# Kernel tuning notes

Measured on AMD Instinct MI355X. Metric: run time of the kernel, lower is better.

Reference implementation:

```python
import jax, jax.numpy as jnp
import numpy as np

# ---- module constants (from init_kwargs) ----
VOXEL_SIZE = np.array([0.1, 0.1, 0.2], np.float32)
PC_RANGE = np.array([0.0, -40.0, -3.0, 70.4, 40.0, 1.0], np.float32)
MAX_PTS = 10            # max_points_in_voxel
MAX_VOX = 40000         # max_voxel_num (hard voxelization cap per sample)
GRID = np.round((PC_RANGE[3:] - PC_RANGE[:3]) / VOXEL_SIZE).astype(np.int32)  # [704,800,20] (x,y,z)
BIG = int(GRID[0]) * int(GRID[1]) * int(GRID[2])

PC_MIN = jnp.asarray(PC_RANGE[:3])
VSIZE = jnp.asarray(VOXEL_SIZE)
GRID_J = jnp.asarray(GRID)

B = 8
N_PER_B = 120000


def setup_inputs() -> dict:
    key = jax.random.key(0)
    k1, = jax.random.split(key, 1)
    u = jax.random.uniform(k1, (B * N_PER_B, 4), dtype=jnp.float32)
    # place points inside (and slightly around) pc_range
    x = u[:, 0] * 72.0 - 0.5
    y = u[:, 1] * 82.0 - 41.0
    z = u[:, 2] * 4.4 - 3.2
    inten = u[:, 3]
    bs_idx = jnp.repeat(jnp.arange(B, dtype=jnp.float32), N_PER_B)
    points = jnp.stack([bs_idx, x, y, z, inten], axis=1)  # [960000, 5]
    return {"points": points, "batch_size": B}


def _voxelize_one(pts):
    """Hard voxelization of one point cloud pts [N,4] -> fixed-size buffers.
    Faithful to first-come voxel ordering and per-voxel point caps."""
    N = pts.shape[0]
    idxs = jnp.arange(N, dtype=jnp.int32)
    xyz = pts[:, :3]
    c = jnp.floor((xyz - PC_MIN) / VSIZE).astype(jnp.int32)  # [N,3] (x,y,z)
    valid = jnp.all((c >= 0) & (c < GRID_J), axis=1)
    lid = (c[:, 2] * GRID[1] + c[:, 1]) * GRID[0] + c[:, 0]  # z-major linear id
    lid = jnp.where(valid, lid, BIG)

    order = jnp.argsort(lid)            # stable: within a voxel, original order kept
    lid_s = lid[order]
    is_new = jnp.concatenate([jnp.ones((1,), bool), lid_s[1:] != lid_s[:-1]])
    gid = jnp.cumsum(is_new.astype(jnp.int32)) - 1           # group id per sorted point
    starts = jax.lax.cummax(jnp.where(is_new, idxs, 0))      # group start position
    pos = idxs - starts                                      # rank inside its voxel

    g_lid = jax.ops.segment_min(lid_s, gid, num_segments=N)
    g_valid = g_lid < BIG
    first_orig = jax.ops.segment_min(order.astype(jnp.int32), gid, num_segments=N)
    # voxel slot = first-appearance rank (invalid/empty groups pushed to the end)
    first_key = jnp.where(g_valid, first_orig, N + idxs)
    perm = jnp.argsort(first_key)
    slot = jnp.zeros(N, jnp.int32).at[perm].set(idxs)

    pslot = slot[gid]
    keep = g_valid[gid] & (pslot < MAX_VOX) & (pos < MAX_PTS)
    sslot = jnp.where(keep, pslot, MAX_VOX)   # overflow bucket, sliced off
    spos = jnp.where(keep, pos, 0)
    voxels = jnp.zeros((MAX_VOX + 1, MAX_PTS, pts.shape[1]), pts.dtype)
    voxels = voxels.at[sslot, spos].set(pts[order])[:MAX_VOX]

    gcount = jax.ops.segment_sum(keep.astype(jnp.int32), gid, num_segments=N)
    gslot = jnp.where(g_valid & (slot < MAX_VOX), slot, MAX_VOX)
    num_points = jnp.zeros(MAX_VOX + 1, jnp.int32).at[gslot].set(gcount)[:MAX_VOX]

    cs = c[order]
    gz = jax.ops.segment_min(cs[:, 2], gid, num_segments=N)
    gy = jax.ops.segment_min(cs[:, 1], gid, num_segments=N)
    gx = jax.ops.segment_min(cs[:, 0], gid, num_segments=N)
    coors = jnp.full((MAX_VOX + 1, 3), -1, jnp.int32)
    coors = coors.at[gslot].set(jnp.stack([gz, gy, gx], axis=1))[:MAX_VOX]  # (z,y,x)
    return voxels, num_points, coors


def reference(points, batch_size):
    feats = points[:, 1:]
    n_per_b = feats.shape[0] // batch_size  # points constructed contiguously per sample
    pts = feats.reshape(batch_size, n_per_b, feats.shape[1])
    voxels_b, num_b, coors_b = jax.vmap(_voxelize_one)(pts)
    voxels = voxels_b.reshape(batch_size * MAX_VOX, MAX_PTS, feats.shape[1])
    num_points = num_b.reshape(-1)
    batch_col = jnp.repeat(jnp.arange(batch_size, dtype=jnp.int32), MAX_VOX)[:, None]
    coors_batch = jnp.concatenate([batch_col, coors_b.reshape(-1, 3)], axis=1)  # [b,z,y,x]
    grid_size = jnp.asarray(GRID)
    return voxels, num_points, coors_batch, grid_size
```

## Files before the change

### kernel.cpp

```cpp
#include <hip/hip_runtime.h>

#define NB        8
#define NPB       120000
#define NPTS      (NB * NPB)
#define MAX_PTS   10
#define MAX_VOX   40000
#define GX        704
#define GY        800
#define GZ        20
#define CELLS     (GX * GY * GZ)
#define WPB       (CELLS / 32)

#define HC2       (1 << 15)
#define HMASK2    (HC2 - 1)
#define NSLOT2    (NB * HC2)

#define TILES     469
#define TILES_PAD 512
#define MBCAP     8192
#define MTILE     2048

#define EMPTY64   0xFFFFFFFFFFFFFFFFull

#define OUT_VOX   0LL
#define OUT_NUM   12800000LL
#define OUT_COOR  13120000LL
#define OUT_GRID  14400000LL

typedef float f4v __attribute__((ext_vector_type(4)));

__device__ __forceinline__ bool point_cell(const float* __restrict__ p,
                                           int& cx, int& cy, int& cz) {
    cx = (int)floorf((p[1] - 0.0f)   / 0.1f);
    cy = (int)floorf((p[2] - (-40.0f)) / 0.1f);
    cz = (int)floorf((p[3] - (-3.0f))  / 0.2f);
    return (cx >= 0) & (cx < GX) & (cy >= 0) & (cy < GY) & (cz >= 0) & (cz < GZ);
}

__device__ __forceinline__ unsigned cell_hash(int lid) {
    return (((unsigned)lid * 2654435761u) >> 17) & HMASK2;
}

__global__ void k_init(float* __restrict__ out, uint4* __restrict__ bm4,
                       ulonglong2* __restrict__ slab2, unsigned* __restrict__ mcount) {
    int t = blockIdx.x * blockDim.x + threadIdx.x;
    int stride = gridDim.x * blockDim.x;
    uint4 z4 = make_uint4(0u, 0u, 0u, 0u);
    for (int i = t; i < NB * WPB / 4; i += stride) bm4[i] = z4;
    ulonglong2 e2; e2.x = EMPTY64; e2.y = EMPTY64;
    if (t < NSLOT2 / 2) slab2[t] = e2;
    f4v z = {0.f, 0.f, 0.f, 0.f};
    f4v* vox = (f4v*)(out + OUT_VOX);
    for (int j = t; j < 3200000; j += stride)
        __builtin_nontemporal_store(z, vox + j);
    if (t < NB) mcount[t * 16] = 0u;
    if (t == 0) {
        out[OUT_GRID + 0] = 704.f;
        out[OUT_GRID + 1] = 800.f;
        out[OUT_GRID + 2] = 20.f;
    }
}

__global__ void k_phase1(const float* __restrict__ pts, unsigned* __restrict__ bm,
                         unsigned long long* __restrict__ slabB,
                         unsigned char* __restrict__ flag, int* __restrict__ lid32) {
    int b = blockIdx.x & 7;
    int idx = (blockIdx.x >> 3) * 256 + threadIdx.x;
    if (idx >= NPB) return;
    int g = b * NPB + idx;
    const float* p = pts + (long long)g * 5;
    int cx, cy, cz;
    if (!point_cell(p, cx, cy, cz)) { flag[g] = 0; lid32[g] = -1; return; }
    int lid = (cz * GY + cy) * GX + cx;
    lid32[g] = lid;
    unsigned mask = 1u << (lid & 31);
    unsigned old = atomicOr(&bm[b * WPB + (lid >> 5)], mask);
    if ((old & mask) == 0u) {
        flag[g] = 1;
    } else {
        flag[g] = 0;
        unsigned long long key = ((unsigned long long)(unsigned)lid << 32)
                               | (unsigned long long)(unsigned)idx;
        unsigned long long* base = slabB + (size_t)b * HC2;
        unsigned h = cell_hash(lid);
        while (true) {
            unsigned long long oo = atomicMin(base + h, key);
            if (oo == EMPTY64) break;
            if ((oo >> 32) == (key >> 32)) break;
            if (oo > key) key = oo;
            h = (h + 1) & HMASK2;
        }
    }
}

__global__ void k_phase2(const int* __restrict__ lid32, unsigned char* __restrict__ flag,
                         unsigned long long* __restrict__ slabB) {
    int b = blockIdx.x & 7;
    int idx = (blockIdx.x >> 3) * 256 + threadIdx.x;
    if (idx >= NPB) return;
    int g = b * NPB + idx;
    if (flag[g] != 1) return;
    int lid = lid32[g];
    unsigned long long* base = slabB + (size_t)b * HC2;
    unsigned h = cell_hash(lid);
    while (true) {
        unsigned long long cur = base[h];
        if (cur == EMPTY64) break;
        if ((unsigned)(cur >> 32) == (unsigned)lid) {
            unsigned long long key = ((unsigned long long)(unsigned)lid << 32)
                                   | (unsigned long long)(unsigned)idx;
            unsigned long long old = atomicMin(&base[h], key);
            unsigned omin = (unsigned)old;
            if (omin < (unsigned)idx) {
                flag[g] = 0;
                flag[b * NPB + (int)omin] = 1;
            }
            break;
        }
        h = (h + 1) & HMASK2;
    }
}

__global__ void k_count(const unsigned* __restrict__ flag32, int* __restrict__ tileSum) {
    int w = blockIdx.x * 4 + ((int)threadIdx.x >> 6);
    int lane = threadIdx.x & 63;
    int b = w & 7;
    int tile = w >> 3;
    int i = tile * 64 + lane;
    unsigned x = (i < NPB / 4) ? flag32[b * (NPB / 4) + i] : 0u;
    int s = (int)((x * 0x01010101u) >> 24);
    #pragma unroll
    for (int off = 32; off; off >>= 1) s += __shfl_down(s, off);
    if (lane == 0) tileSum[b * TILES_PAD + tile] = s;
}

__global__ void k_finish(const float* __restrict__ pts, const int* __restrict__ lid32,
                         const unsigned char* __restrict__ flag,
                         const int* __restrict__ tileSum,
                         const unsigned long long* __restrict__ slabB,
                         float* __restrict__ out, unsigned short* __restrict__ slotOf,
                         int2* __restrict__ mlist, unsigned* __restrict__ mcount) {
    int b = blockIdx.x & 7;
    int tile = blockIdx.x >> 3;
    int t = threadIdx.x;

    __shared__ int sc[256];
    __shared__ int soff[TILES_PAD];
    int v0 = (2 * t     < TILES) ? tileSum[b * TILES_PAD + 2 * t]     : 0;
    int v1 = (2 * t + 1 < TILES) ? tileSum[b * TILES_PAD + 2 * t + 1] : 0;
    int w = v0 + v1;
    sc[t] = w;
    __syncthreads();
    for (int off = 1; off < 256; off <<= 1) {
        int x = sc[t];
        if (t >= off) x += sc[t - off];
        __syncthreads();
        sc[t] = x;
        __syncthreads();
    }
    int e = sc[t] - w;
    soff[2 * t] = e;
    soff[2 * t + 1] = e + v0;
    __syncthreads();

    int idx = tile * 256 + t;
    int g = b * NPB + idx;
    int f = (idx < NPB) ? (int)flag[g] : 0;
    sc[t] = f;
    __syncthreads();
    for (int off = 1; off < 256; off <<= 1) {
        int x = sc[t];
        if (t >= off) x += sc[t - off];
        __syncthreads();
        sc[t] = x;
        __syncthreads();
    }
    int rank = sc[t] - f;

    if (idx >= NPB) return;
    int lid = lid32[g];
    if (lid < 0) return;

    if (f) {
        int slot = soff[tile] + rank;
        slotOf[g] = (unsigned short)(slot < 65535 ? slot : 65535);
        if (slot >= MAX_VOX) return;
        unsigned ul = (unsigned)lid;
        unsigned cx = ul % (unsigned)GX;
        unsigned tt = ul / (unsigned)GX;
        unsigned cy = tt % (unsigned)GY;
        unsigned cz = tt / (unsigned)GY;
        long long r = (long long)b * MAX_VOX + slot;
        ((float4*)(out + OUT_COOR))[r] = make_float4((float)b, (float)cz, (float)cy, (float)cx);
        out[OUT_NUM + r] = 1.f;
        const float* p = pts + (long long)g * 5;
        ((float4*)(out + OUT_VOX))[r * MAX_PTS] = make_float4(p[1], p[2], p[3], p[4]);
    } else {
        const unsigned long long* base = slabB + (size_t)b * HC2;
        unsigned h = cell_hash(lid);
        unsigned long long cur;
        while (true) {
            cur = base[h];
            if ((unsigned)(cur >> 32) == (unsigned)lid) break;
            h = (h + 1) & HMASK2;
        }
        unsigned minidx = (unsigned)cur;
        unsigned m = atomicAdd(&mcount[b * 16], 1u);
        if (m < MBCAP) mlist[(size_t)b * MBCAP + m] = make_int2((int)minidx, idx);
    }
}

__global__ void k_multi(const float* __restrict__ pts,
                        const int2* __restrict__ mlist, const unsigned* __restrict__ mcount,
                        const unsigned short* __restrict__ slotOf,
                        float* __restrict__ out) {
    int b = blockIdx.y;
    unsigned n = mcount[b * 16];
    if (n > MBCAP) n = MBCAP;
    unsigned t = blockIdx.x * blockDim.x + threadIdx.x;
    const int2* lst = mlist + (size_t)b * MBCAP;
    bool active = (t < n);
    int2 e = active ? lst[t] : make_int2(-1, -1);
    int pos = 1;
    int same = 0;
    __shared__ int2 sm[MTILE];
    for (unsigned chunk = 0; chunk < n; chunk += MTILE) {
        unsigned m = n - chunk;
        if (m > MTILE) m = MTILE;
        for (unsigned i = threadIdx.x; i < m; i += 256)
            sm[i] = lst[chunk + i];
        __syncthreads();
        if (active) {
            #pragma unroll 4
            for (unsigned j = 0; j < m; j++) {
                int2 o = sm[j];
                if (o.x == e.x) { same++; if (o.y < e.y) pos++; }
            }
        }
        __syncthreads();
    }
    if (!active) return;
    int slot = (int)slotOf[(size_t)b * NPB + e.x];
    if (slot >= MAX_VOX) return;
    if (pos == 1) {
        int cnt = same + 1;
        out[OUT_NUM + (long long)b * MAX_VOX + slot] =
            (float)(cnt < MAX_PTS ? cnt : MAX_PTS);
    }
    if (pos >= MAX_PTS) return;
    const float* p = pts + ((long long)b * NPB + e.y) * 5;
    ((float4*)(out + OUT_VOX))[(long long)(b * MAX_VOX + slot) * MAX_PTS + pos] =
        make_float4(p[1], p[2], p[3], p[4]);
}

extern "C" void kernel_launch(void* const* d_in, const int* in_sizes, int n_in,
                              void* d_out, int out_size, void* d_ws, size_t ws_size,
                              hipStream_t stream) {
    const float* pts = (const float*)d_in[0];
    float* out = (float*)d_out;

    char* w = (char*)d_ws;
    unsigned* bm = (unsigned*)w;              w += (size_t)NB * WPB * 4;
    unsigned long long* slabB = (unsigned long long*)w;
    w += (size_t)NSLOT2 * 8;
    int2* mlist = (int2*)w;  w += (size_t)NB * MBCAP * 8;
    int* lid32 = (int*)w;    w += (size_t)NPTS * 4;
    int* tileSum = (int*)w;  w += (size_t)NB * TILES_PAD * 4;
    unsigned* mcount = (unsigned*)w; w += (size_t)NB * 16 * 4;
    unsigned short* slotOf = (unsigned short*)w; w += (size_t)NPTS * 2;
    unsigned char* flag = (unsigned char*)w;  w += (size_t)NPTS;

    const int PB = TILES * NB;
    k_init<<<dim3(2048), dim3(256), 0, stream>>>(out, (uint4*)bm, (ulonglong2*)slabB, mcount);
    k_phase1<<<dim3(PB), dim3(256), 0, stream>>>(pts, bm, slabB, flag, lid32);
    k_phase2<<<dim3(PB), dim3(256), 0, stream>>>(lid32, flag, slabB);
    k_count<<<dim3((TILES * NB + 3) / 4), dim3(256), 0, stream>>>((const unsigned*)flag, tileSum);
    k_finish<<<dim3(PB), dim3(256), 0, stream>>>(pts, lid32, flag, tileSum, slabB,
                                                 out, slotOf, mlist, mcount);
    k_multi<<<dim3(MBCAP / 256, NB), dim3(256), 0, stream>>>(pts, mlist, mcount, slotOf, out);
}
```

Before: 164.1 us.

## Replace voxel occupancy bitmap with non-atomic two-level hash election tables

The full-grid occupancy bitmap and its atomicOr are replaced. Each valid point writes its index into a per-sample hash table with plain stores, and the surviving entry is checked against lid32 to pick one representative per cell. Colliding points go to a second, smaller table, and anything left over falls back to the existing atomicMin slab. This removes the large bitmap zeroing pass and most of the atomics. Cell computation is also folded into the init kernel. The cost is an extra kernel launch, scattered writes into about 10 MB of tables, and more complex flag-state logic in phase2.

```diff
diff --git a/kernel.cpp b/kernel.cpp
--- a/kernel.cpp
+++ b/kernel.cpp
@@ -8,8 +8,11 @@
 #define GX        704
 #define GY        800
 #define GZ        20
-#define CELLS     (GX * GY * GZ)
-#define WPB       (CELLS / 32)
+
+#define T0        (1 << 18)
+#define T0MASK    (T0 - 1)
+#define T1        (1 << 16)
+#define T1MASK    (T1 - 1)
 
 #define HC2       (1 << 15)
 #define HMASK2    (HC2 - 1)
@@ -37,22 +40,55 @@
     return (cx >= 0) & (cx < GX) & (cy >= 0) & (cy < GY) & (cz >= 0) & (cz < GZ);
 }
 
-__device__ __forceinline__ unsigned cell_hash(int lid) {
+__device__ __forceinline__ unsigned hash0(int lid) {
+    return (((unsigned)lid * 2654435761u) >> 14) & T0MASK;
+}
+__device__ __forceinline__ unsigned hash1(int lid) {
+    return (((unsigned)lid * 0x9E3779B1u) >> 16) & T1MASK;
+}
+__device__ __forceinline__ unsigned slab_hash(int lid) {
     return (((unsigned)lid * 2654435761u) >> 17) & HMASK2;
 }
 
-__global__ void k_init(float* __restrict__ out, uint4* __restrict__ bm4,
-                       ulonglong2* __restrict__ slab2, unsigned* __restrict__ mcount) {
-    int t = blockIdx.x * blockDim.x + threadIdx.x;
-    int stride = gridDim.x * blockDim.x;
-    uint4 z4 = make_uint4(0u, 0u, 0u, 0u);
-    for (int i = t; i < NB * WPB / 4; i += stride) bm4[i] = z4;
-    ulonglong2 e2; e2.x = EMPTY64; e2.y = EMPTY64;
-    if (t < NSLOT2 / 2) slab2[t] = e2;
+__device__ __forceinline__ void slab_insert(unsigned long long* __restrict__ base,
+                                            int lid, int idx) {
+    unsigned long long key = ((unsigned long long)(unsigned)lid << 32)
+                           | (unsigned long long)(unsigned)idx;
+    unsigned h = slab_hash(lid);
+    while (true) {
+        unsigned long long oo = atomicMin(base + h, key);
+        if (oo == EMPTY64) break;
+        if ((oo >> 32) == (key >> 32)) break;
+        if (oo > key) key = oo;
+        h = (h + 1) & HMASK2;
+    }
+}
+
+__global__ void k_init(const float* __restrict__ pts, float* __restrict__ out,
+                       ulonglong2* __restrict__ slab2, unsigned* __restrict__ tbl0,
+                       int* __restrict__ lid32, unsigned* __restrict__ mcount) {
+    int b = blockIdx.x & 7;
+    int idx = (blockIdx.x >> 3) * 256 + threadIdx.x;
+    if (idx < NPB) {
+        int g = b * NPB + idx;
+        const float* p = pts + (long long)g * 5;
+        int cx, cy, cz;
+        if (point_cell(p, cx, cy, cz)) {
+            int lid = (cz * GY + cy) * GX + cx;
+            lid32[g] = lid;
+            tbl0[b * T0 + hash0(lid)] = (unsigned)idx;
+        } else {
+            lid32[g] = -1;
+        }
+    }
+    int t = blockIdx.x * 256 + threadIdx.x;
+    int stride = gridDim.x * 256;
     f4v z = {0.f, 0.f, 0.f, 0.f};
     f4v* vox = (f4v*)(out + OUT_VOX);
     for (int j = t; j < 3200000; j += stride)
         __builtin_nontemporal_store(z, vox + j);
+    ulonglong2 e2; e2.x = EMPTY64; e2.y = EMPTY64;
+    if (t < NSLOT2 / 2) slab2[t] = e2;
     if (t < NB) mcount[t * 16] = 0u;
     if (t == 0) {
         out[OUT_GRID + 0] = 704.f;
@@ -61,63 +97,81 @@
     }
 }
 
-__global__ void k_phase1(const float* __restrict__ pts, unsigned* __restrict__ bm,
-                         unsigned long long* __restrict__ slabB,
-                         unsigned char* __restrict__ flag, int* __restrict__ lid32) {
+__global__ void k_l0(const int* __restrict__ lid32, const unsigned* __restrict__ tbl0,
+                     unsigned* __restrict__ tbl1, unsigned char* __restrict__ flag,
+                     unsigned long long* __restrict__ slabB) {
     int b = blockIdx.x & 7;
     int idx = (blockIdx.x >> 3) * 256 + threadIdx.x;
     if (idx >= NPB) return;
     int g = b * NPB + idx;
-    const float* p = pts + (long long)g * 5;
-    int cx, cy, cz;
-    if (!point_cell(p, cx, cy, cz)) { flag[g] = 0; lid32[g] = -1; return; }
-    int lid = (cz * GY + cy) * GX + cx;
-    lid32[g] = lid;
-    unsigned mask = 1u << (lid & 31);
-    unsigned old = atomicOr(&bm[b * WPB + (lid >> 5)], mask);
-    if ((old & mask) == 0u) {
-        flag[g] = 1;
+    int lid = lid32[g];
+    if (lid < 0) { flag[g] = 0; return; }
+    unsigned w = tbl0[b * T0 + hash0(lid)];
+    if (lid32[b * NPB + (int)w] == lid) {
+        if (w == (unsigned)idx) flag[g] = 1;
+        else { flag[g] = 0; slab_insert(slabB + (size_t)b * HC2, lid, idx); }
     } else {
-        flag[g] = 0;
-        unsigned long long key = ((unsigned long long)(unsigned)lid << 32)
-                               | (unsigned long long)(unsigned)idx;
-        unsigned long long* base = slabB + (size_t)b * HC2;
-        unsigned h = cell_hash(lid);
-        while (true) {
-            unsigned long long oo = atomicMin(base + h, key);
-            if (oo == EMPTY64) break;
-            if ((oo >> 32) == (key >> 32)) break;
-            if (oo > key) key = oo;
-            h = (h + 1) & HMASK2;
-        }
-    }
-}
-
-__global__ void k_phase2(const int* __restrict__ lid32, unsigned char* __restrict__ flag,
-                         unsigned long long* __restrict__ slabB) {
+        tbl1[b * T1 + hash1(lid)] = (unsigned)idx;
+        flag[g] = 2;
+    }
+}
+
+__global__ void k_l1(const int* __restrict__ lid32, const unsigned* __restrict__ tbl1,
+                     unsigned char* __restrict__ flag,
+                     unsigned long long* __restrict__ slabB) {
     int b = blockIdx.x & 7;
     int idx = (blockIdx.x >> 3) * 256 + threadIdx.x;
     if (idx >= NPB) return;
     int g = b * NPB + idx;
-    if (flag[g] != 1) return;
+    if (flag[g] != 2) return;
+    int lid = lid32[g];
+    unsigned w = tbl1[b * T1 + hash1(lid)];
+    if (lid32[b * NPB + (int)w] == lid) {
+        if (w == (unsigned)idx) flag[g] = 1;
+        else { flag[g] = 0; slab_insert(slabB + (size_t)b * HC2, lid, idx); }
+    } else {
+        slab_insert(slabB + (size_t)b * HC2, lid, idx);
+        flag[g] = 3;
+    }
+}
+
+__global__ void k_phase2(const int* __restrict__ lid32, unsigned char* __restrict__ flag,
+                         unsigned long long* __restrict__ slabB) {
+    int b = blockIdx.x & 7;
+    int idx = (blockIdx.x >> 3) * 256 + threadIdx.x;
+    if (idx >= NPB) return;
+    int g = b * NPB + idx;
+    unsigned char fl = flag[g];
+    if (fl != 1 && fl != 3) return;
     int lid = lid32[g];
     unsigned long long* base = slabB + (size_t)b * HC2;
-    unsigned h = cell_hash(lid);
-    while (true) {
-        unsigned long long cur = base[h];
-        if (cur == EMPTY64) break;
-        if ((unsigned)(cur >> 32) == (unsigned)lid) {
-            unsigned long long key = ((unsigned long long)(unsigned)lid << 32)
-                                   | (unsigned long long)(unsigned)idx;
-            unsigned long long old = atomicMin(&base[h], key);
-            unsigned omin = (unsigned)old;
-            if (omin < (unsigned)idx) {
-                flag[g] = 0;
-                flag[b * NPB + (int)omin] = 1;
+    unsigned h = slab_hash(lid);
+    if (fl == 1) {
+        while (true) {
+            unsigned long long cur = base[h];
+            if (cur == EMPTY64) break;
+            if ((unsigned)(cur >> 32) == (unsigned)lid) {
+                unsigned long long key = ((unsigned long long)(unsigned)lid << 32)
+                                       | (unsigned long long)(unsigned)idx;
+                unsigned long long old = atomicMin(&base[h], key);
+                unsigned omin = (unsigned)old;
+                if (omin < (unsigned)idx) {
+                    flag[g] = 0;
+                    flag[b * NPB + (int)omin] = 1;
+                }
+                break;
             }
-            break;
-        }
-        h = (h + 1) & HMASK2;
+            h = (h + 1) & HMASK2;
+        }
+    } else {
+        while (true) {
+            unsigned long long cur = base[h];
+            if ((unsigned)(cur >> 32) == (unsigned)lid) {
+                flag[g] = ((unsigned)cur == (unsigned)idx) ? 1 : 0;
+                break;
+            }
+            h = (h + 1) & HMASK2;
+        }
     }
 }
 
@@ -197,7 +251,7 @@
         ((float4*)(out + OUT_VOX))[r * MAX_PTS] = make_float4(p[1], p[2], p[3], p[4]);
     } else {
         const unsigned long long* base = slabB + (size_t)b * HC2;
-        unsigned h = cell_hash(lid);
+        unsigned h = slab_hash(lid);
         unsigned long long cur;
         while (true) {
             cur = base[h];
@@ -260,7 +314,8 @@
     float* out = (float*)d_out;
 
     char* w = (char*)d_ws;
-    unsigned* bm = (unsigned*)w;              w += (size_t)NB * WPB * 4;
+    unsigned* tbl0 = (unsigned*)w;            w += (size_t)NB * T0 * 4;
+    unsigned* tbl1 = (unsigned*)w;            w += (size_t)NB * T1 * 4;
     unsigned long long* slabB = (unsigned long long*)w;
     w += (size_t)NSLOT2 * 8;
     int2* mlist = (int2*)w;  w += (size_t)NB * MBCAP * 8;
@@ -271,8 +326,9 @@
     unsigned char* flag = (unsigned char*)w;  w += (size_t)NPTS;
 
     const int PB = TILES * NB;
-    k_init<<<dim3(2048), dim3(256), 0, stream>>>(out, (uint4*)bm, (ulonglong2*)slabB, mcount);
-    k_phase1<<<dim3(PB), dim3(256), 0, stream>>>(pts, bm, slabB, flag, lid32);
+    k_init<<<dim3(PB), dim3(256), 0, stream>>>(pts, out, (ulonglong2*)slabB, tbl0, lid32, mcount);
+    k_l0<<<dim3(PB), dim3(256), 0, stream>>>(lid32, tbl0, tbl1, flag, slabB);
+    k_l1<<<dim3(PB), dim3(256), 0, stream>>>(lid32, tbl1, flag, slabB);
     k_phase2<<<dim3(PB), dim3(256), 0, stream>>>(lid32, flag, slabB);
     k_count<<<dim3((TILES * NB + 3) / 4), dim3(256), 0, stream>>>((const unsigned*)flag, tileSum);
     k_finish<<<dim3(PB), dim3(256), 0, stream>>>(pts, lid32, flag, tileSum, slabB,
```

New measurement: 153.1 us. 1.07x faster.
